# Performance work log

Measured on AMD Instinct MI355X. Metric: run time of the kernel, lower is better.

## Reference

```python
import jax, jax.numpy as jnp
import numpy as np

D = 256       # d_model
H = 8         # nhead
W = 2048      # num windows (single drop level)
T = 64        # max_tokens per window (drop_info['num_sampled_tokens'][dl])
FILL = 48
N = W * FILL  # total voxels


def setup_inputs() -> dict:
    key = jax.random.key(0)
    k0, k1, k2, k3 = jax.random.split(key, 4)
    voxel_feat = jax.random.normal(k0, (N, D), jnp.float32)
    pos_embed = jax.random.normal(k1, (N, D), jnp.float32)
    # nn.MultiheadAttention params: packed in_proj [3D, D] and out_proj [D, D]
    in_proj_w = jax.random.normal(k2, (3 * D, D), jnp.float32) * (1.0 / np.sqrt(D))
    in_proj_b = jnp.zeros((3 * D,), jnp.float32)
    out_proj_w = jax.random.normal(k3, (D, D), jnp.float32) * (1.0 / np.sqrt(D))
    out_proj_b = jnp.zeros((D,), jnp.float32)
    # each voxel assigned a (window, in-window-slot) pair; slots unique per window
    window_idx = (jnp.arange(N) // FILL).astype(jnp.int32)
    slot_idx = (jnp.arange(N) % FILL).astype(jnp.int32)
    return {
        'voxel_feat': voxel_feat, 'pos_embed': pos_embed,
        'in_proj_w': in_proj_w, 'in_proj_b': in_proj_b,
        'out_proj_w': out_proj_w, 'out_proj_b': out_proj_b,
        'window_idx': window_idx, 'slot_idx': slot_idx,
        'num_windows': W, 'max_tokens': T,
    }


def reference(voxel_feat, pos_embed, in_proj_w, in_proj_b, out_proj_w, out_proj_b,
              window_idx, slot_idx, num_windows, max_tokens):
    Dm = voxel_feat.shape[-1]
    hd = Dm // H  # head dim
    P = num_windows * max_tokens  # padded token count
    valid = window_idx.astype(jnp.int32) * max_tokens + slot_idx.astype(jnp.int32)

    # scatter voxels into padded dense windows
    feat = jnp.zeros((P, Dm), voxel_feat.dtype).at[valid].set(voxel_feat)
    pos = jnp.ones((P, Dm), voxel_feat.dtype).at[valid].set(pos_embed)
    kmask = jnp.zeros((P,), bool).at[valid].set(True).reshape(num_windows, max_tokens)  # True = valid key
    feat = feat.reshape(num_windows, max_tokens, Dm)
    pos = pos.reshape(num_windows, max_tokens, Dm)

    # MHA: q = k = feat + pos, v = feat (torch nn.MultiheadAttention math)
    Wq, Wk, Wv = jnp.split(in_proj_w, 3, axis=0)
    bq, bk, bv = jnp.split(in_proj_b, 3, axis=0)
    qk_in = feat + pos
    q = (qk_in @ Wq.T + bq).reshape(num_windows, max_tokens, H, hd)
    k = (qk_in @ Wk.T + bk).reshape(num_windows, max_tokens, H, hd)
    v = (feat @ Wv.T + bv).reshape(num_windows, max_tokens, H, hd)

    scale = 1.0 / np.sqrt(hd)
    scores = jnp.einsum('wqhd,wkhd->whqk', q, k) * scale  # [W, H, T, T]
    scores = jnp.where(kmask[:, None, None, :], scores, -jnp.inf)  # key_padding_mask
    attn = jax.nn.softmax(scores, axis=-1)
    out = jnp.einsum('whqk,wkhd->wqhd', attn, v).reshape(P, Dm)
    out = out @ out_proj_w.T + out_proj_b

    # gather valid tokens back to per-voxel output (padded rows dropped, as in original)
    return out[valid]
```

## Files before the change

kernel.cpp:

```cpp
#include <hip/hip_runtime.h>

#define DD 256
#define TT 64
#define WW 2048

typedef unsigned short u16;
typedef __attribute__((ext_vector_type(8))) __bf16 bf8_t;
typedef __attribute__((ext_vector_type(4))) float  f32x4;

#define XSW(tok, col) ((tok) * 256 + ((col) ^ (((tok) & 7) << 3)))

__device__ __forceinline__ u16 f2bf(float x) {
  union { float f; unsigned u; } c; c.f = x;
  unsigned r = c.u + 0x7FFFu + ((c.u >> 16) & 1u);
  return (u16)(r >> 16);
}
__device__ __forceinline__ int pack2(float a, float b) {
  return (int)((unsigned)f2bf(a) | ((unsigned)f2bf(b) << 16));
}

__global__ void prep_weights(const float* __restrict__ inw, const float* __restrict__ outw,
                             u16* __restrict__ fragW, u16* __restrict__ fragWo) {
  int i = blockIdx.x * blockDim.x + threadIdx.x;
  int row = i >> 8, k = i & 255;
  int l  = (((k >> 3) & 3) << 4) | (row & 15);
  int j  = k & 7;
  int kt = k >> 5;
  if (i < 768 * 256)
    fragW[((size_t)(kt * 48 + (row >> 4)) * 64 + l) * 8 + j] = f2bf(inw[i]);
  if (i < 256 * 256)
    fragWo[((size_t)(kt * 16 + (row >> 4)) * 64 + l) * 8 + j] = f2bf(outw[i]);
}

__global__ void build_slots(const int* __restrict__ widx, const int* __restrict__ sidx,
                            int* __restrict__ wslots, int n) {
  int i = blockIdx.x * blockDim.x + threadIdx.x;
  if (i < n) wslots[widx[i] * TT + sidx[i]] = i;
}

__global__ __launch_bounds__(768, 3) void qkv_gemm(
    const float* __restrict__ feat, const float* __restrict__ pos,
    const u16* __restrict__ fragW, const float* __restrict__ inb,
    const int* __restrict__ widx, const int* __restrict__ sidx,
    u16* __restrict__ qc, u16* __restrict__ kc, u16* __restrict__ vt) {

  __shared__ u16 Xqk[TT * 264];
  __shared__ u16 Xv[TT * 264];
  __shared__ u16 cb[TT * 520];

  const int t    = threadIdx.x;
  const int wv   = t >> 6;
  const int lane = t & 63;
  const int g    = lane >> 4;
  const int l16  = lane & 15;
  const int m0   = blockIdx.x * 64;

  if (t < 512) {
    int vox = t >> 3, seg = t & 7;
    const float4* fp = (const float4*)(feat + (size_t)(m0 + vox) * DD + seg * 32);
    const float4* pp = (const float4*)(pos  + (size_t)(m0 + vox) * DD + seg * 32);
    float4 f[8], p[8];
#pragma unroll
    for (int j = 0; j < 8; ++j) { f[j] = fp[j]; p[j] = pp[j]; }
    const float* ff = (const float*)f;
    const float* pf = (const float*)p;
#pragma unroll
    for (int c = 0; c < 4; ++c) {
      union { u16 u[8]; bf8_t v; } rq, rv;
#pragma unroll
      for (int j = 0; j < 8; ++j) {
        float fv = ff[c * 8 + j];
        rq.u[j] = f2bf(fv + pf[c * 8 + j]);
        rv.u[j] = f2bf(fv);
      }
      *(bf8_t*)&Xqk[vox * 264 + seg * 32 + c * 8] = rq.v;
      *(bf8_t*)&Xv[vox * 264 + seg * 32 + c * 8]  = rv.v;
    }
  }
  __syncthreads();

  const bool isV   = (wv >= 8);
  const u16* Xsrc  = isV ? Xv : Xqk;
  const int rtbase = isV ? (32 + (wv - 8) * 4) : (wv * 4);

  const f32x4 zf = {0.f, 0.f, 0.f, 0.f};
  f32x4 acc[4][4];
#pragma unroll
  for (int mt = 0; mt < 4; ++mt)
#pragma unroll
    for (int nt = 0; nt < 4; ++nt) acc[mt][nt] = zf;

  bf8_t wf[4];
#pragma unroll
  for (int nt = 0; nt < 4; ++nt)
    wf[nt] = *(const bf8_t*)&fragW[((size_t)(rtbase + nt) * 64 + lane) * 8];

#pragma unroll
  for (int kt = 0; kt < 8; ++kt) {
    bf8_t wn[4];
    if (kt < 7) {
#pragma unroll
      for (int nt = 0; nt < 4; ++nt)
        wn[nt] = *(const bf8_t*)&fragW[((size_t)((kt + 1) * 48 + rtbase + nt) * 64 + lane) * 8];
    }
    bf8_t xa[4];
#pragma unroll
    for (int mt = 0; mt < 4; ++mt)
      xa[mt] = *(const bf8_t*)&Xsrc[(mt * 16 + l16) * 264 + kt * 32 + g * 8];

    if (!isV) {
#pragma unroll
      for (int nt = 0; nt < 4; ++nt)
#pragma unroll
        for (int mt = 0; mt < 4; ++mt)
          acc[mt][nt] = __builtin_amdgcn_mfma_f32_16x16x32_bf16(xa[mt], wf[nt], acc[mt][nt], 0, 0, 0);
    } else {
#pragma unroll
      for (int mt = 0; mt < 4; ++mt)
#pragma unroll
        for (int nt = 0; nt < 4; ++nt)
          acc[mt][nt] = __builtin_amdgcn_mfma_f32_16x16x32_bf16(wf[mt], xa[nt], acc[mt][nt], 0, 0, 0);
    }
    if (kt < 7) {
#pragma unroll
      for (int nt = 0; nt < 4; ++nt) wf[nt] = wn[nt];
    }
  }

  if (!isV) {
#pragma unroll
    for (int nt = 0; nt < 4; ++nt) {
      float b = inb[wv * 64 + nt * 16 + l16];
#pragma unroll
      for (int mt = 0; mt < 4; ++mt)
#pragma unroll
        for (int r = 0; r < 4; ++r)
          cb[(mt * 16 + 4 * g + r) * 520 + wv * 64 + nt * 16 + l16] = f2bf(acc[mt][nt][r] + b);
    }
  } else {
#pragma unroll
    for (int nt = 0; nt < 4; ++nt) {
      int vx = m0 + nt * 16 + l16;
      size_t bw_ = (size_t)widx[vx] * (DD * TT) + sidx[vx];
#pragma unroll
      for (int mt = 0; mt < 4; ++mt)
#pragma unroll
        for (int r = 0; r < 4; ++r) {
          int vd = (wv - 8) * 64 + mt * 16 + 4 * g + r;
          vt[bw_ + (size_t)vd * TT] = f2bf(acc[mt][nt][r] + inb[512 + vd]);
        }
    }
  }
  __syncthreads();

#pragma unroll
  for (int r = 0; r < 6; ++r) {
    int c = r * 768 + t;
    if (c < 4096) {
      int vox = c >> 6, col = (c & 63) * 8;
      bf8_t v = *(const bf8_t*)&cb[vox * 520 + col];
      if (col < 256) *(bf8_t*)&qc[(size_t)(m0 + vox) * DD + col] = v;
      else           *(bf8_t*)&kc[(size_t)(m0 + vox) * DD + col - 256] = v;
    }
  }
}

__global__ __launch_bounds__(256, 4) void attn_out(
    const u16* __restrict__ qc, const u16* __restrict__ kc, const u16* __restrict__ vt,
    const u16* __restrict__ fragWo, const float* __restrict__ outb,
    const int* __restrict__ wslots, float* __restrict__ out) {

  __shared__ int tl[TT];
  __shared__ u16 ab[TT * 256];

  const int t    = threadIdx.x;
  const int wv   = t >> 6;
  const int lane = t & 63;
  const int g    = lane >> 4;
  const int l16  = lane & 15;
  const int w    = blockIdx.x;

  if (t < TT) tl[t] = wslots[w * TT + t];
  __syncthreads();

  const f32x4 zf = {0.f, 0.f, 0.f, 0.f};

  bool vm[4][4];
#pragma unroll
  for (int mt = 0; mt < 4; ++mt)
#pragma unroll
    for (int r = 0; r < 4; ++r) vm[mt][r] = (tl[mt * 16 + 4 * g + r] >= 0);

#pragma unroll 1
  for (int hh = 0; hh < 2; ++hh) {
    const int h = wv * 2 + hh;

    bf8_t akf[4], bqf[4];
#pragma unroll
    for (int mt = 0; mt < 4; ++mt) {
      int row = tl[mt * 16 + l16]; row = row < 0 ? 0 : row;
      akf[mt] = *(const bf8_t*)&kc[(size_t)row * DD + h * 32 + g * 8];
    }
#pragma unroll
    for (int nt = 0; nt < 4; ++nt) {
      int row = tl[nt * 16 + l16]; row = row < 0 ? 0 : row;
      bqf[nt] = *(const bf8_t*)&qc[(size_t)row * DD + h * 32 + g * 8];
    }

    f32x4 sa[4][4];
#pragma unroll
    for (int mt = 0; mt < 4; ++mt)
#pragma unroll
      for (int nt = 0; nt < 4; ++nt)
        sa[mt][nt] = __builtin_amdgcn_mfma_f32_16x16x32_bf16(akf[mt], bqf[nt], zf, 0, 0, 0);

    const float scale = 0.17677669529663687f;
    int pk[4][4][2];
#pragma unroll
    for (int nt = 0; nt < 4; ++nt) {
      float sv[4][4];
      float m = -3e38f;
#pragma unroll
      for (int mt = 0; mt < 4; ++mt)
#pragma unroll
        for (int r = 0; r < 4; ++r) {
          float s = vm[mt][r] ? sa[mt][nt][r] * scale : -3e38f;
          sv[mt][r] = s;
          m = fmaxf(m, s);
        }
      m = fmaxf(m, __shfl_xor(m, 16, 64));
      m = fmaxf(m, __shfl_xor(m, 32, 64));
      float sum = 0.f;
#pragma unroll
      for (int mt = 0; mt < 4; ++mt)
#pragma unroll
        for (int r = 0; r < 4; ++r) {
          float pv = vm[mt][r] ? __expf(sv[mt][r] - m) : 0.f;
          sv[mt][r] = pv;
          sum += pv;
        }
      sum += __shfl_xor(sum, 16, 64);
      sum += __shfl_xor(sum, 32, 64);
      float inv = sum > 0.f ? 1.f / sum : 0.f;
#pragma unroll
      for (int mt = 0; mt < 4; ++mt)
#pragma unroll
        for (int rp = 0; rp < 2; ++rp)
          pk[mt][nt][rp] = pack2(sv[mt][2 * rp] * inv, sv[mt][2 * rp + 1] * inv);
    }

    bf8_t avf[2][2];
#pragma unroll
    for (int md = 0; md < 2; ++md)
#pragma unroll
      for (int kk = 0; kk < 2; ++kk)
        avf[md][kk] = *(const bf8_t*)&vt[(size_t)w * (DD * TT) +
                                        (size_t)(h * 32 + md * 16 + l16) * TT + kk * 32 + g * 8];

    f32x4 oa[2][4];
#pragma unroll
    for (int md = 0; md < 2; ++md)
#pragma unroll
      for (int nt = 0; nt < 4; ++nt) oa[md][nt] = zf;

#pragma unroll
    for (int kk = 0; kk < 2; ++kk) {
#pragma unroll
      for (int nt = 0; nt < 4; ++nt) {
        union { int wd[4]; bf8_t v; } bu;
#pragma unroll
        for (int wd = 0; wd < 4; ++wd) {
          int src = l16 + 16 * (2 * (g & 1) + (wd >> 1));
          int lo = __shfl(pk[2 * kk + 0][nt][wd & 1], src, 64);
          int hi = __shfl(pk[2 * kk + 1][nt][wd & 1], src, 64);
          bu.wd[wd] = (g & 2) ? hi : lo;
        }
#pragma unroll
        for (int md = 0; md < 2; ++md)
          oa[md][nt] = __builtin_amdgcn_mfma_f32_16x16x32_bf16(avf[md][kk], bu.v, oa[md][nt], 0, 0, 0);
      }
    }

#pragma unroll
    for (int md = 0; md < 2; ++md)
#pragma unroll
      for (int nt = 0; nt < 4; ++nt) {
        int w0 = pack2(oa[md][nt][0], oa[md][nt][1]);
        int w1 = pack2(oa[md][nt][2], oa[md][nt][3]);
        *(int2*)&ab[XSW(nt * 16 + l16, h * 32 + md * 16 + 4 * g)] = make_int2(w0, w1);
      }
  }
  __syncthreads();

  f32x4 fa[4][4];
#pragma unroll
  for (int mt = 0; mt < 4; ++mt)
#pragma unroll
    for (int nt = 0; nt < 4; ++nt) fa[mt][nt] = zf;

  bf8_t bwf[4];
#pragma unroll
  for (int nt = 0; nt < 4; ++nt)
    bwf[nt] = *(const bf8_t*)&fragWo[((size_t)(wv * 4 + nt) * 64 + lane) * 8];

#pragma unroll
  for (int kk = 0; kk < 8; ++kk) {
    bf8_t bwn[4];
    if (kk < 7) {
#pragma unroll
      for (int nt = 0; nt < 4; ++nt)
        bwn[nt] = *(const bf8_t*)&fragWo[((size_t)((kk + 1) * 16 + wv * 4 + nt) * 64 + lane) * 8];
    }
    bf8_t aa[4];
#pragma unroll
    for (int mt = 0; mt < 4; ++mt)
      aa[mt] = *(const bf8_t*)&ab[XSW(mt * 16 + l16, kk * 32 + g * 8)];
#pragma unroll
    for (int nt = 0; nt < 4; ++nt)
#pragma unroll
      for (int mt = 0; mt < 4; ++mt)
        fa[mt][nt] = __builtin_amdgcn_mfma_f32_16x16x32_bf16(aa[mt], bwf[nt], fa[mt][nt], 0, 0, 0);
    if (kk < 7) {
#pragma unroll
      for (int nt = 0; nt < 4; ++nt) bwf[nt] = bwn[nt];
    }
  }

#pragma unroll
  for (int nt = 0; nt < 4; ++nt) {
    float ob = outb[wv * 64 + nt * 16 + l16];
#pragma unroll
    for (int mt = 0; mt < 4; ++mt)
#pragma unroll
      for (int r = 0; r < 4; ++r) {
        int row = tl[mt * 16 + 4 * g + r];
        if (row >= 0)
          out[(size_t)row * DD + wv * 64 + nt * 16 + l16] = fa[mt][nt][r] + ob;
      }
  }
}

extern "C" void kernel_launch(void* const* d_in, const int* in_sizes, int n_in,
                              void* d_out, int out_size, void* d_ws, size_t ws_size,
                              hipStream_t stream) {
  (void)n_in; (void)out_size; (void)ws_size;
  const float* feat = (const float*)d_in[0];
  const float* pos  = (const float*)d_in[1];
  const float* inw  = (const float*)d_in[2];
  const float* inb  = (const float*)d_in[3];
  const float* outw = (const float*)d_in[4];
  const float* outb = (const float*)d_in[5];
  const int*   widx = (const int*)d_in[6];
  const int*   sidx = (const int*)d_in[7];
  const int N = in_sizes[0] / DD;

  char* ws = (char*)d_ws;
  u16* fragW  = (u16*)ws;
  u16* fragWo = (u16*)(ws + 393216);
  int* wslots = (int*)(ws + 393216 + 131072);
  size_t off  = 1048576;
  u16* qc = (u16*)(ws + off); off += (size_t)N * DD * 2;
  u16* kc = (u16*)(ws + off); off += (size_t)N * DD * 2;
  u16* vt = (u16*)(ws + off);

  hipMemsetAsync(wslots, 0xFF, WW * TT * sizeof(int), stream);
  prep_weights<<<768, 256, 0, stream>>>(inw, outw, fragW, fragWo);
  build_slots<<<(N + 255) / 256, 256, 0, stream>>>(widx, sidx, wslots, N);
  qkv_gemm<<<N / 64, 768, 0, stream>>>(feat, pos, fragW, inb, widx, sidx, qc, kc, vt);
  attn_out<<<WW, 256, 0, stream>>>(qc, kc, vt, fragWo, outb, wslots, (float*)d_out);
}
```

Measured before the change: 312.0 us.

## Split QKV projection into three 256-thread blocks per voxel tile

The fused QKV GEMM block of 768 threads (12 waves) is split across a grid dimension of 3, so each 256-thread block computes only Q, K, or V for a 64-voxel tile. Each block keeps only one bf16 input tile in shared memory and reuses it as the output staging buffer, which cuts LDS per block and should allow more blocks to be resident. In exchange, feat is read three times and pos twice from global memory, and the Q/K blocks add an extra barrier.

Result: faster. 260.4 us (-16.5%).

```diff
diff --git a/kernel.cpp b/kernel.cpp
--- a/kernel.cpp
+++ b/kernel.cpp
@@ -38,50 +38,60 @@
   if (i < n) wslots[widx[i] * TT + sidx[i]] = i;
 }
 
-__global__ __launch_bounds__(768, 3) void qkv_gemm(
+__global__ __launch_bounds__(256, 3) void qkv_gemm(
     const float* __restrict__ feat, const float* __restrict__ pos,
     const u16* __restrict__ fragW, const float* __restrict__ inb,
     const int* __restrict__ widx, const int* __restrict__ sidx,
     u16* __restrict__ qc, u16* __restrict__ kc, u16* __restrict__ vt) {
 
-  __shared__ u16 Xqk[TT * 264];
-  __shared__ u16 Xv[TT * 264];
-  __shared__ u16 cb[TT * 520];
+  __shared__ u16 XB[TT * 264];
 
   const int t    = threadIdx.x;
   const int wv   = t >> 6;
   const int lane = t & 63;
   const int g    = lane >> 4;
   const int l16  = lane & 15;
-  const int m0   = blockIdx.x * 64;
-
-  if (t < 512) {
-    int vox = t >> 3, seg = t & 7;
-    const float4* fp = (const float4*)(feat + (size_t)(m0 + vox) * DD + seg * 32);
-    const float4* pp = (const float4*)(pos  + (size_t)(m0 + vox) * DD + seg * 32);
-    float4 f[8], p[8];
-#pragma unroll
-    for (int j = 0; j < 8; ++j) { f[j] = fp[j]; p[j] = pp[j]; }
-    const float* ff = (const float*)f;
-    const float* pf = (const float*)p;
-#pragma unroll
-    for (int c = 0; c < 4; ++c) {
-      union { u16 u[8]; bf8_t v; } rq, rv;
-#pragma unroll
-      for (int j = 0; j < 8; ++j) {
-        float fv = ff[c * 8 + j];
-        rq.u[j] = f2bf(fv + pf[c * 8 + j]);
-        rv.u[j] = f2bf(fv);
+  const int p    = blockIdx.x;
+  const int m0   = blockIdx.y * 64;
+
+  {
+    const int vox  = t >> 2;
+    const int dblk = (t & 3) * 64;
+#pragma unroll
+    for (int c2 = 0; c2 < 2; ++c2) {
+      const int d0 = dblk + c2 * 32;
+      const float4* fp = (const float4*)(feat + (size_t)(m0 + vox) * DD + d0);
+      float4 f[8];
+#pragma unroll
+      for (int j = 0; j < 8; ++j) f[j] = fp[j];
+      const float* ff = (const float*)f;
+      if (p < 2) {
+        const float4* pp = (const float4*)(pos + (size_t)(m0 + vox) * DD + d0);
+        float4 q[8];
+#pragma unroll
+        for (int j = 0; j < 8; ++j) q[j] = pp[j];
+        const float* pf = (const float*)q;
+#pragma unroll
+        for (int c = 0; c < 4; ++c) {
+          union { u16 u[8]; bf8_t v; } r;
+#pragma unroll
+          for (int j = 0; j < 8; ++j) r.u[j] = f2bf(ff[c * 8 + j] + pf[c * 8 + j]);
+          *(bf8_t*)&XB[vox * 264 + d0 + c * 8] = r.v;
+        }
+      } else {
+#pragma unroll
+        for (int c = 0; c < 4; ++c) {
+          union { u16 u[8]; bf8_t v; } r;
+#pragma unroll
+          for (int j = 0; j < 8; ++j) r.u[j] = f2bf(ff[c * 8 + j]);
+          *(bf8_t*)&XB[vox * 264 + d0 + c * 8] = r.v;
+        }
       }
-      *(bf8_t*)&Xqk[vox * 264 + seg * 32 + c * 8] = rq.v;
-      *(bf8_t*)&Xv[vox * 264 + seg * 32 + c * 8]  = rv.v;
     }
   }
   __syncthreads();
 
-  const bool isV   = (wv >= 8);
-  const u16* Xsrc  = isV ? Xv : Xqk;
-  const int rtbase = isV ? (32 + (wv - 8) * 4) : (wv * 4);
+  const int rtb = p * 16 + wv * 4;
 
   const f32x4 zf = {0.f, 0.f, 0.f, 0.f};
   f32x4 acc[4][4];
@@ -93,7 +103,7 @@
   bf8_t wf[4];
 #pragma unroll
   for (int nt = 0; nt < 4; ++nt)
-    wf[nt] = *(const bf8_t*)&fragW[((size_t)(rtbase + nt) * 64 + lane) * 8];
+    wf[nt] = *(const bf8_t*)&fragW[((size_t)(rtb + nt) * 64 + lane) * 8];
 
 #pragma unroll
   for (int kt = 0; kt < 8; ++kt) {
@@ -101,14 +111,14 @@
     if (kt < 7) {
 #pragma unroll
       for (int nt = 0; nt < 4; ++nt)
-        wn[nt] = *(const bf8_t*)&fragW[((size_t)((kt + 1) * 48 + rtbase + nt) * 64 + lane) * 8];
+        wn[nt] = *(const bf8_t*)&fragW[((size_t)((kt + 1) * 48 + rtb + nt) * 64 + lane) * 8];
     }
     bf8_t xa[4];
 #pragma unroll
     for (int mt = 0; mt < 4; ++mt)
-      xa[mt] = *(const bf8_t*)&Xsrc[(mt * 16 + l16) * 264 + kt * 32 + g * 8];
-
-    if (!isV) {
+      xa[mt] = *(const bf8_t*)&XB[(mt * 16 + l16) * 264 + kt * 32 + g * 8];
+
+    if (p < 2) {
 #pragma unroll
       for (int nt = 0; nt < 4; ++nt)
 #pragma unroll
@@ -127,15 +137,24 @@
     }
   }
 
-  if (!isV) {
+  if (p < 2) {
+    __syncthreads();
 #pragma unroll
     for (int nt = 0; nt < 4; ++nt) {
-      float b = inb[wv * 64 + nt * 16 + l16];
+      float b = inb[p * 256 + wv * 64 + nt * 16 + l16];
 #pragma unroll
       for (int mt = 0; mt < 4; ++mt)
 #pragma unroll
         for (int r = 0; r < 4; ++r)
-          cb[(mt * 16 + 4 * g + r) * 520 + wv * 64 + nt * 16 + l16] = f2bf(acc[mt][nt][r] + b);
+          XB[(mt * 16 + 4 * g + r) * 264 + wv * 64 + nt * 16 + l16] = f2bf(acc[mt][nt][r] + b);
+    }
+    __syncthreads();
+    u16* dst = p ? kc : qc;
+#pragma unroll
+    for (int it = 0; it < 8; ++it) {
+      int i = it * 256 + t;
+      int row = i >> 5, col = (i & 31) * 8;
+      *(bf8_t*)&dst[(size_t)(m0 + row) * DD + col] = *(const bf8_t*)&XB[row * 264 + col];
     }
   } else {
 #pragma unroll
@@ -146,21 +165,9 @@
       for (int mt = 0; mt < 4; ++mt)
 #pragma unroll
         for (int r = 0; r < 4; ++r) {
-          int vd = (wv - 8) * 64 + mt * 16 + 4 * g + r;
+          int vd = wv * 64 + mt * 16 + 4 * g + r;
           vt[bw_ + (size_t)vd * TT] = f2bf(acc[mt][nt][r] + inb[512 + vd]);
         }
-    }
-  }
-  __syncthreads();
-
-#pragma unroll
-  for (int r = 0; r < 6; ++r) {
-    int c = r * 768 + t;
-    if (c < 4096) {
-      int vox = c >> 6, col = (c & 63) * 8;
-      bf8_t v = *(const bf8_t*)&cb[vox * 520 + col];
-      if (col < 256) *(bf8_t*)&qc[(size_t)(m0 + vox) * DD + col] = v;
-      else           *(bf8_t*)&kc[(size_t)(m0 + vox) * DD + col - 256] = v;
     }
   }
 }
@@ -366,6 +373,6 @@
   hipMemsetAsync(wslots, 0xFF, WW * TT * sizeof(int), stream);
   prep_weights<<<768, 256, 0, stream>>>(inw, outw, fragW, fragWo);
   build_slots<<<(N + 255) / 256, 256, 0, stream>>>(widx, sidx, wslots, N);
-  qkv_gemm<<<N / 64, 768, 0, stream>>>(feat, pos, fragW, inb, widx, sidx, qc, kc, vt);
+  qkv_gemm<<<dim3(3, N / 64), 256, 0, stream>>>(feat, pos, fragW, inb, widx, sidx, qc, kc, vt);
   attn_out<<<WW, 256, 0, stream>>>(qc, kc, vt, fragWo, outb, wslots, (float*)d_out);
 }
```
